# Optimization experiments

Hardware: AMD Instinct MI355X
Metric: run time of the kernel (lower is better)

## Reference

```python
import jax, jax.numpy as jnp
import numpy as np

N = 30000      # nodes
E = 480000     # edges
H = 128        # hidden_nf
NQ = 7         # qubits
D = 2 ** NQ    # 128, quantum state dim == embedding_size
NL = 2         # block n_layers (QGCL layers)
QL = 2         # quantum circuit layers inside each QGCL
NORM = 100.0   # normalization_factor ('sum' aggregation)
NORM_CONST = 1.0


def _cnot_perm_indices(n):
    # Composed permutation for CNOT(0,1)...CNOT(n-2,n-1), CNOT(n-1,0).
    # PennyLane convention: wire 0 is the most significant bit.
    idx = np.arange(2 ** n)
    pairs = [(i, i + 1) for i in range(n - 1)] + [(n - 1, 0)]
    g = None
    for c, t in pairs:
        cb = (idx >> (n - 1 - c)) & 1
        f = idx ^ (cb << (n - 1 - t))  # flip target bit if control set (involution)
        g = f if g is None else g[f]
    return g

_CNOT_G = jnp.asarray(_cnot_perm_indices(NQ))


def _quantum_states(q_in, coeffs, A_re, A_im):
    """Vectorized VQC over all nodes. q_in [N,D] real -> [N,D] complex state."""
    norm = jnp.sqrt(jnp.sum(q_in ** 2, axis=1, keepdims=True) + 1e-12)
    s = (q_in / norm).astype(jnp.complex64)  # normalized initial state per node
    I = jnp.eye(D, dtype=jnp.complex64)
    for j in range(QL):
        # Cayley transform -> unitary
        A = (A_re[j] + 1j * A_im[j]).astype(jnp.complex64)
        A = A + A.conj().T
        q = (A - 1j * I) @ jnp.linalg.inv(A + 1j * I)
        # single-qubit layer: RY(b) @ RX(a) on every qubit -> kron power
        a, b = coeffs[j, 0].astype(jnp.complex64), coeffs[j, 1].astype(jnp.complex64)
        ca, sa = jnp.cos(a / 2), jnp.sin(a / 2)
        cb, sb = jnp.cos(b / 2), jnp.sin(b / 2)
        RX = jnp.stack([jnp.stack([ca, -1j * sa]), jnp.stack([-1j * sa, ca])])
        RY = jnp.stack([jnp.stack([cb, -sb]), jnp.stack([sb, cb])])
        G = RY @ RX
        Gk = G
        for _ in range(NQ - 1):
            Gk = jnp.kron(Gk, G)
        s = s @ q.T            # QubitUnitary
        s = s @ Gk.T           # RX/RY on all qubits
        s = s[:, _CNOT_G]      # CNOT ring (pure permutation)
    return s


def setup_inputs() -> dict:
    key = jax.random.key(0)
    ks = jax.random.split(key, 20)
    return {
        "h": jax.random.normal(ks[0], (N, H), jnp.float32),
        "x": jax.random.normal(ks[1], (N, 3), jnp.float32),
        "edge_index": jax.random.randint(ks[2], (2, E), 0, N, jnp.int32),
        "edge_attr": jax.random.normal(ks[3], (E, 1), jnp.float32),
        "e_w1": jax.random.normal(ks[4], (NL, 2 * H + 2, H), jnp.float32) * 0.05,
        "e_b1": jnp.zeros((NL, H), jnp.float32),
        "e_w2": jax.random.normal(ks[5], (NL, H, H), jnp.float32) * 0.05,
        "e_b2": jnp.zeros((NL, H), jnp.float32),
        "enc_w": jax.random.normal(ks[6], (NL, 2 * H, D), jnp.float32) * 0.05,
        "enc_b": jnp.zeros((NL, D), jnp.float32),
        "coeffs": jax.random.normal(ks[7], (NL, QL, 2), jnp.float32) * 0.1,
        "A_re": jax.random.normal(ks[8], (NL, QL, D, D), jnp.float32) * 0.01,
        "A_im": jax.random.normal(ks[9], (NL, QL, D, D), jnp.float32) * 0.01,
        "dec_w": jax.random.normal(ks[10], (NL, D, H), jnp.float32) * 0.05,
        "dec_b": jnp.zeros((NL, H), jnp.float32),
        "c_w1": jax.random.normal(ks[11], (2 * H + 2, H), jnp.float32) * 0.05,
        "c_b1": jnp.zeros((H,), jnp.float32),
        "c_w2": jax.random.normal(ks[12], (H, H), jnp.float32) * 0.05,
        "c_b2": jnp.zeros((H,), jnp.float32),
        "c_w3": jax.random.normal(ks[13], (H, 1), jnp.float32) * 0.001,  # xavier gain=0.001
    }


def reference(h, x, edge_index, edge_attr, e_w1, e_b1, e_w2, e_b2, enc_w, enc_b,
              coeffs, A_re, A_im, dec_w, dec_b, c_w1, c_b1, c_w2, c_b2, c_w3):
    row, col = edge_index[0], edge_index[1]
    # coord2diff
    diff = x[row] - x[col]
    radial = jnp.sum(diff ** 2, axis=1, keepdims=True)     # [E,1] (used as 'distances')
    coord_diff = diff / (jnp.sqrt(radial + 1e-8) + NORM_CONST)
    eattr = jnp.concatenate([radial, edge_attr], axis=1)   # [E,2]

    for l in range(NL):  # QGCL layers
        m = jnp.concatenate([h[row], h[col], eattr], axis=1)       # [E, 2H+2]
        m = jax.nn.silu(m @ e_w1[l] + e_b1[l])
        m = jax.nn.silu(m @ e_w2[l] + e_b2[l])                     # edge messages mij
        agg = jax.ops.segment_sum(m, row, num_segments=N) / NORM   # scatter-add
        q_in = jnp.concatenate([h, agg], axis=1) @ enc_w[l] + enc_b[l]
        # quantum part is detached in the original (torch .detach + re-tensor)
        qs = jax.lax.stop_gradient(
            _quantum_states(q_in, coeffs[l], A_re[l], A_im[l]))
        h = h + qs.real.astype(h.dtype) @ dec_w[l] + dec_b[l]

    # EquivariantUpdate (tanh=False)
    t = jnp.concatenate([h[row], h[col], eattr], axis=1)
    t = jax.nn.silu(t @ c_w1 + c_b1)
    t = jax.nn.silu(t @ c_w2 + c_b2)
    t = t @ c_w3                                                   # [E,1]
    trans = coord_diff * t
    x = x + jax.ops.segment_sum(trans, row, num_segments=N) / NORM
    return h, x
```

## Files before the change

### kernel.cpp

```cpp
#include <hip/hip_runtime.h>
#include <math.h>

#define N_NODES 30000
#define N_EDGES 480000
#define HDIM 128
#define EPB 64
#define AS 296
#define NAS 264
#define MS 136

typedef __attribute__((ext_vector_type(8))) short short8b;
typedef __attribute__((ext_vector_type(4))) float f32x4;

__device__ __forceinline__ float silu_f(float v) {
  return v / (1.0f + __expf(-v));
}

__device__ __forceinline__ unsigned short f2bf(float f) {
  unsigned int u = __float_as_uint(f);
  unsigned int r = u + 0x7fffu + ((u >> 16) & 1u);
  return (unsigned short)(r >> 16);
}

__global__ void init_out_kernel(const float* __restrict__ h,
                                const float* __restrict__ x,
                                float* __restrict__ out) {
  int idx = blockIdx.x * 256 + threadIdx.x;
  out[idx] = h[idx];
  if (idx < N_NODES * 3) out[N_NODES * HDIM + idx] = x[idx];
}

__global__ void h_to_bf_kernel(const float* __restrict__ h,
                               ushort* __restrict__ hbf) {
  int idx = blockIdx.x * 256 + threadIdx.x;
  float4 v = ((const float4*)h)[idx];
  ushort4 o;
  o.x = f2bf(v.x); o.y = f2bf(v.y); o.z = f2bf(v.z); o.w = f2bf(v.w);
  ((ushort4*)hbf)[idx] = o;
}

__global__ void convert_w_kernel(const float* __restrict__ W,
                                 ushort* __restrict__ dst, int Kreal, int KT) {
  int idx = blockIdx.x * 256 + threadIdx.x;
  if (idx >= KT * 4096) return;
  int kt = idx >> 12, rem = idx & 4095, n = rem >> 5, kk = rem & 31;
  int k = kt * 32 + kk;
  float v = (k < Kreal) ? W[(size_t)k * HDIM + n] : 0.0f;
  dst[idx] = f2bf(v);
}

__global__ void count_kernel(const int* __restrict__ ei, int* __restrict__ cursor) {
  int e = blockIdx.x * 256 + threadIdx.x;
  atomicAdd(&cursor[ei[e]], 1);
}

__global__ __launch_bounds__(1024) void scan_kernel(int* __restrict__ cursor,
                                                    int* __restrict__ cstart) {
  __shared__ int sums[1024];
  const int tid = threadIdx.x;
  const int base = tid * 30;
  int local[30];
  int s = 0;
#pragma unroll
  for (int j = 0; j < 30; ++j) {
    int idx = base + j;
    int d = (idx < N_NODES) ? cursor[idx] : 0;
    local[j] = s;
    s += d;
  }
  sums[tid] = s;
  __syncthreads();
  for (int off = 1; off < 1024; off <<= 1) {
    int add = (tid >= off) ? sums[tid - off] : 0;
    __syncthreads();
    sums[tid] += add;
    __syncthreads();
  }
  int excl = (tid == 0) ? 0 : sums[tid - 1];
#pragma unroll
  for (int j = 0; j < 30; ++j) {
    int idx = base + j;
    if (idx < N_NODES) {
      int v = excl + local[j];
      cursor[idx] = v;
      cstart[idx] = v;
    }
  }
}

__global__ void fill_kernel(const int* __restrict__ ei, int* __restrict__ cursor,
                            int* __restrict__ elist) {
  int e = blockIdx.x * 256 + threadIdx.x;
  int r = ei[e];
  int pos = atomicAdd(&cursor[r], 1);
  elist[pos] = e;
}

__global__ void perm_kernel(int* __restrict__ g) {
  int i = threadIdx.x;
  int v = i;
  const int cs[7] = {6, 5, 4, 3, 2, 1, 0};
  const int ts[7] = {0, 6, 5, 4, 3, 2, 1};
#pragma unroll
  for (int p = 0; p < 7; ++p) {
    int cb = (v >> (6 - cs[p])) & 1;
    v = v ^ (cb << (6 - ts[p]));
  }
  g[i] = v;
}

__global__ void ns_init_kernel(const float* __restrict__ Are,
                               const float* __restrict__ Aim,
                               float2* __restrict__ X) {
  int lj = blockIdx.y;
  int idx = blockIdx.x * 256 + threadIdx.x;
  int r = idx >> 7, c = idx & 127;
  const float* are = Are + (size_t)lj * 16384;
  const float* aim = Aim + (size_t)lj * 16384;
  float re = are[r * 128 + c] + are[c * 128 + r];
  float im = aim[r * 128 + c] - aim[c * 128 + r];
  if (r == c) im -= 1.0f;
  X[(size_t)lj * 16384 + idx] = make_float2(re, im);
}

__global__ void ns_bx_kernel(const float* __restrict__ Are,
                             const float* __restrict__ Aim,
                             const float2* __restrict__ X,
                             float2* __restrict__ T) {
  int lj = blockIdx.y;
  int idx = blockIdx.x * 256 + threadIdx.x;
  int r = idx >> 7, c = idx & 127;
  const float* are = Are + (size_t)lj * 16384;
  const float* aim = Aim + (size_t)lj * 16384;
  const float2* x = X + (size_t)lj * 16384;
  float2 acc = make_float2(0.f, 0.f);
  for (int k = 0; k < 128; ++k) {
    float re = are[r * 128 + k] + are[k * 128 + r];
    float im = aim[r * 128 + k] - aim[k * 128 + r];
    if (k == r) im += 1.0f;
    float2 b = x[k * 128 + c];
    acc.x += re * b.x - im * b.y;
    acc.y += re * b.y + im * b.x;
  }
  T[(size_t)lj * 16384 + idx] = acc;
}

__global__ void ns_upd_kernel(const float2* __restrict__ X,
                              const float2* __restrict__ T,
                              float2* __restrict__ Xn) {
  int lj = blockIdx.y;
  int idx = blockIdx.x * 256 + threadIdx.x;
  int r = idx >> 7, c = idx & 127;
  const float2* x = X + (size_t)lj * 16384;
  const float2* t = T + (size_t)lj * 16384;
  float2 acc = make_float2(0.f, 0.f);
  for (int k = 0; k < 128; ++k) {
    float2 a = x[r * 128 + k];
    float2 b = t[k * 128 + c];
    acc.x += a.x * b.x - a.y * b.y;
    acc.y += a.x * b.y + a.y * b.x;
  }
  float2 xc = x[r * 128 + c];
  Xn[(size_t)lj * 16384 + idx] = make_float2(2.f * xc.x - acc.x, 2.f * xc.y - acc.y);
}

__global__ void qmat_kernel(const float* __restrict__ Are,
                            const float* __restrict__ Aim,
                            const float2* __restrict__ binvg,
                            float2* __restrict__ qm) {
  int lj = blockIdx.y;
  int idx = blockIdx.x * 256 + threadIdx.x;
  int r = idx >> 7, c = idx & 127;
  const float* are = Are + (size_t)lj * 16384;
  const float* aim = Aim + (size_t)lj * 16384;
  const float2* binv = binvg + (size_t)lj * 16384;
  float2 acc = make_float2(0.f, 0.f);
  for (int k = 0; k < 128; ++k) {
    float re = are[r * 128 + k] + are[k * 128 + r];
    float im = aim[r * 128 + k] - aim[k * 128 + r];
    if (k == r) im -= 1.0f;
    float2 b = binv[k * 128 + c];
    acc.x += re * b.x - im * b.y;
    acc.y += re * b.y + im * b.x;
  }
  qm[(size_t)lj * 16384 + idx] = acc;
}

__global__ void gk_kernel(const float* __restrict__ coeffs,
                          float2* __restrict__ gkm) {
  int lj = blockIdx.y;
  float a = coeffs[lj * 2 + 0], b = coeffs[lj * 2 + 1];
  float ca = cosf(0.5f * a), sa = sinf(0.5f * a);
  float cb = cosf(0.5f * b), sb = sinf(0.5f * b);
  float2 G[2][2];
  G[0][0] = make_float2(cb * ca, sb * sa);
  G[0][1] = make_float2(-sb * ca, -cb * sa);
  G[1][0] = make_float2(sb * ca, -cb * sa);
  G[1][1] = make_float2(cb * ca, -sb * sa);
  int idx = blockIdx.x * 256 + threadIdx.x;
  int r = idx >> 7, c = idx & 127;
  float2 acc = make_float2(1.f, 0.f);
#pragma unroll
  for (int bit = 6; bit >= 0; --bit) {
    float2 g = G[(r >> bit) & 1][(c >> bit) & 1];
    acc = make_float2(acc.x * g.x - acc.y * g.y, acc.x * g.y + acc.y * g.x);
  }
  gkm[(size_t)lj * 16384 + idx] = acc;
}

__global__ void nj_kernel(const float2* __restrict__ qm,
                          const float2* __restrict__ gkm,
                          const int* __restrict__ g,
                          float2* __restrict__ njm) {
  int lj = blockIdx.y;
  int idx = blockIdx.x * 256 + threadIdx.x;
  int i = idx >> 7, c = idx & 127;
  int gc = g[c];
  const float2* q = qm + (size_t)lj * 16384;
  const float2* gk = gkm + (size_t)lj * 16384;
  float2 acc = make_float2(0.f, 0.f);
  for (int k = 0; k < 128; ++k) {
    float2 qa = q[k * 128 + i];
    float2 gb = gk[gc * 128 + k];
    acc.x += qa.x * gb.x - qa.y * gb.y;
    acc.y += qa.x * gb.y + qa.y * gb.x;
  }
  njm[(size_t)lj * 16384 + idx] = acc;
}

__global__ void compose_kernel(const float2* __restrict__ njm,
                               float2* __restrict__ um) {
  int l = blockIdx.y;
  int idx = blockIdx.x * 256 + threadIdx.x;
  int i = idx >> 7, c = idx & 127;
  const float2* n0 = njm + (size_t)(l * 2 + 0) * 16384;
  const float2* n1 = njm + (size_t)(l * 2 + 1) * 16384;
  float2 acc = make_float2(0.f, 0.f);
  for (int k = 0; k < 128; ++k) {
    float2 a = n0[i * 128 + k];
    float2 b = n1[k * 128 + c];
    acc.x += a.x * b.x - a.y * b.y;
    acc.y += a.x * b.y + a.y * b.x;
  }
  um[(size_t)l * 16384 + idx] = acc;
}

__global__ void wqd_kernel(const float2* __restrict__ um,
                           const float* __restrict__ decw,
                           float* __restrict__ wqd) {
  int l = blockIdx.y;
  int idx = blockIdx.x * 256 + threadIdx.x;
  int i = idx >> 7, c = idx & 127;
  const float2* u = um + (size_t)l * 16384;
  const float* dw = decw + (size_t)l * 16384;
  float acc = 0.f;
  for (int k = 0; k < 128; ++k) acc += u[i * 128 + k].x * dw[k * 128 + c];
  wqd[(size_t)l * 16384 + idx] = acc;
}

__global__ __launch_bounds__(256, 4) void edge_mfma_kernel(
    const ushort* __restrict__ hbf, const int* __restrict__ ei,
    const float* __restrict__ x, const float* __restrict__ ea,
    const int* __restrict__ elist, const int* __restrict__ cstart,
    const ushort* __restrict__ w1cs, const float* __restrict__ b1,
    const ushort* __restrict__ w2cs, const float* __restrict__ b2,
    float* __restrict__ agg, float* __restrict__ headp) {
  __shared__ ushort A[EPB * AS];
  __shared__ int rows[EPB];
  ushort* m1 = A;
  float* m2 = (float*)A;

  const int tid = threadIdx.x;
  const int lane = tid & 63, wave = tid >> 6;
  const int lrow = lane & 15, lq = lane >> 4;
  const int wbase = wave * 32;
  const int woff0 = (wbase + lrow) * 32 + lq * 8;
  const int woff1 = (wbase + 16 + lrow) * 32 + lq * 8;

  const float b1v[2] = {b1[wbase + lrow], b1[wbase + 16 + lrow]};
  const float b2v[2] = {b2[wbase + lrow], b2[wbase + 16 + lrow]};

  const int i0 = blockIdx.x * EPB;
  {
    const int e = tid >> 2, j = tid & 3;
    const int edge = elist[i0 + e];
    const int r = ei[edge], c = ei[N_EDGES + edge];
    if (j == 0) rows[e] = r;
    const uint4* hr = (const uint4*)(hbf + (size_t)r * HDIM + j * 32);
    const uint4* hc = (const uint4*)(hbf + (size_t)c * HDIM + j * 32);
    uint4* d1 = (uint4*)(A + e * AS + j * 32);
    uint4* d2 = (uint4*)(A + e * AS + 128 + j * 32);
    d1[0] = hr[0]; d1[1] = hr[1]; d1[2] = hr[2]; d1[3] = hr[3];
    d2[0] = hc[0]; d2[1] = hc[1]; d2[2] = hc[2]; d2[3] = hc[3];
    if (j == 3) {
      float dx = x[r * 3 + 0] - x[c * 3 + 0];
      float dy = x[r * 3 + 1] - x[c * 3 + 1];
      float dz = x[r * 3 + 2] - x[c * 3 + 2];
      ushort* dst = A + e * AS;
      dst[256] = f2bf(dx * dx + dy * dy + dz * dz);
      dst[257] = f2bf(ea[edge]);
#pragma unroll
      for (int z = 258; z < 288; ++z) dst[z] = 0;
    }
  }
  __syncthreads();

  f32x4 acc[4][2];
#pragma unroll
  for (int mt = 0; mt < 4; ++mt)
#pragma unroll
    for (int nt = 0; nt < 2; ++nt) acc[mt][nt] = (f32x4){0.f, 0.f, 0.f, 0.f};
  {
    short8b wcur0 = *(const short8b*)(w1cs + woff0);
    short8b wcur1 = *(const short8b*)(w1cs + woff1);
#pragma unroll
    for (int kt = 0; kt < 9; ++kt) {
      short8b wn0, wn1;
      if (kt < 8) {
        wn0 = *(const short8b*)(w1cs + (kt + 1) * 4096 + woff0);
        wn1 = *(const short8b*)(w1cs + (kt + 1) * 4096 + woff1);
      }
      short8b af[4];
#pragma unroll
      for (int mt = 0; mt < 4; ++mt)
        af[mt] = *(const short8b*)(A + (mt * 16 + lrow) * AS + kt * 32 + lq * 8);
#pragma unroll
      for (int mt = 0; mt < 4; ++mt) {
        acc[mt][0] = __builtin_amdgcn_mfma_f32_16x16x32_bf16(af[mt], wcur0, acc[mt][0], 0, 0, 0);
        acc[mt][1] = __builtin_amdgcn_mfma_f32_16x16x32_bf16(af[mt], wcur1, acc[mt][1], 0, 0, 0);
      }
      if (kt < 8) { wcur0 = wn0; wcur1 = wn1; }
    }
  }
  __syncthreads();
#pragma unroll
  for (int mt = 0; mt < 4; ++mt)
#pragma unroll
    for (int nt = 0; nt < 2; ++nt)
#pragma unroll
      for (int r = 0; r < 4; ++r)
        m1[(mt * 16 + lq * 4 + r) * MS + wbase + nt * 16 + lrow] =
            f2bf(silu_f(acc[mt][nt][r] + b1v[nt]));
  __syncthreads();

  f32x4 acc2[4][2];
#pragma unroll
  for (int mt = 0; mt < 4; ++mt)
#pragma unroll
    for (int nt = 0; nt < 2; ++nt) acc2[mt][nt] = (f32x4){0.f, 0.f, 0.f, 0.f};
  {
    short8b wcur0 = *(const short8b*)(w2cs + woff0);
    short8b wcur1 = *(const short8b*)(w2cs + woff1);
#pragma unroll
    for (int kt = 0; kt < 4; ++kt) {
      short8b wn0, wn1;
      if (kt < 3) {
        wn0 = *(const short8b*)(w2cs + (kt + 1) * 4096 + woff0);
        wn1 = *(const short8b*)(w2cs + (kt + 1) * 4096 + woff1);
      }
      short8b af[4];
#pragma unroll
      for (int mt = 0; mt < 4; ++mt)
        af[mt] = *(const short8b*)(m1 + (mt * 16 + lrow) * MS + kt * 32 + lq * 8);
#pragma unroll
      for (int mt = 0; mt < 4; ++mt) {
        acc2[mt][0] = __builtin_amdgcn_mfma_f32_16x16x32_bf16(af[mt], wcur0, acc2[mt][0], 0, 0, 0);
        acc2[mt][1] = __builtin_amdgcn_mfma_f32_16x16x32_bf16(af[mt], wcur1, acc2[mt][1], 0, 0, 0);
      }
      if (kt < 3) { wcur0 = wn0; wcur1 = wn1; }
    }
  }
  __syncthreads();
#pragma unroll
  for (int mt = 0; mt < 4; ++mt)
#pragma unroll
    for (int nt = 0; nt < 2; ++nt)
#pragma unroll
      for (int r = 0; r < 4; ++r)
        m2[(mt * 16 + lq * 4 + r) * MS + wbase + nt * 16 + lrow] =
            silu_f(acc2[mt][nt][r] + b2v[nt]);
  __syncthreads();

  const int e2 = tid & 63, cg = tid >> 6, cb = cg * 32;
  const int r_e = rows[e2];
  const bool leader = (e2 == 0) || (rows[e2 - 1] != r_e);
  if (leader) {
    f32x4 sum[8];
#pragma unroll
    for (int q = 0; q < 8; ++q) sum[q] = *(const f32x4*)(m2 + e2 * MS + cb + q * 4);
    int f = e2 + 1;
    while (f < EPB && rows[f] == r_e) {
#pragma unroll
      for (int q = 0; q < 8; ++q) sum[q] += *(const f32x4*)(m2 + f * MS + cb + q * 4);
      ++f;
    }
    float* dst = (e2 == 0 && cstart[r_e] < i0)
                     ? headp + (size_t)blockIdx.x * HDIM + cb
                     : agg + (size_t)r_e * HDIM + cb;
#pragma unroll
    for (int q = 0; q < 8; ++q) *(f32x4*)(dst + q * 4) = sum[q];
  }
}

__global__ __launch_bounds__(256, 2) void node_mfma_kernel(
    float* __restrict__ out_h, const float* __restrict__ agg,
    const int* __restrict__ cstart, const int* __restrict__ cend,
    const float* __restrict__ headp,
    const ushort* __restrict__ enccs, const float* __restrict__ encb,
    const ushort* __restrict__ wqdcs, const float* __restrict__ decb,
    ushort* __restrict__ hbf) {
  __shared__ ushort A[EPB * NAS];
  __shared__ ushort m1[EPB * MS];
  __shared__ float nbuf[4 * EPB];
  const int tid = threadIdx.x;
  const int n0 = blockIdx.x * EPB;

  const int lane = tid & 63, wave = tid >> 6;
  const int lrow = lane & 15, lq = lane >> 4;
  const int wbase = wave * 32;

  short8b wef[8][2], wqf[4][2];
#pragma unroll
  for (int kt = 0; kt < 8; ++kt)
#pragma unroll
    for (int nt = 0; nt < 2; ++nt)
      wef[kt][nt] = *(const short8b*)(enccs + kt * 4096 + (wbase + nt * 16 + lrow) * 32 + lq * 8);
#pragma unroll
  for (int kt = 0; kt < 4; ++kt)
#pragma unroll
    for (int nt = 0; nt < 2; ++nt)
      wqf[kt][nt] = *(const short8b*)(wqdcs + kt * 4096 + (wbase + nt * 16 + lrow) * 32 + lq * 8);
  const float ebv[2] = {encb[wbase + lrow], encb[wbase + 16 + lrow]};
  const float dbv[2] = {decb[wbase + lrow], decb[wbase + 16 + lrow]};

  {
    const int e = tid >> 2, j = tid & 3;
    int node = n0 + e;
    if (node >= N_NODES) node = N_NODES - 1;
    if (j < 2) {
      const float4* s4 = (const float4*)(out_h + (size_t)node * HDIM + j * 64);
      ushort* dst = A + e * NAS + j * 64;
#pragma unroll
      for (int i = 0; i < 16; ++i) {
        float4 v = s4[i];
        ushort4 o;
        o.x = f2bf(v.x); o.y = f2bf(v.y); o.z = f2bf(v.z); o.w = f2bf(v.w);
        ((ushort4*)dst)[i] = o;
      }
    } else {
      const int s = cstart[node], en = cend[node];
      const bool hasAgg = en > s;
      const float4* a4 = (const float4*)(agg + (size_t)node * HDIM + (j - 2) * 64);
      const int bb0 = (s >> 6) + 1;
      const int bb1 = hasAgg ? ((en - 1) >> 6) : 0;
      ushort* dst = A + e * NAS + 128 + (j - 2) * 64;
#pragma unroll
      for (int i = 0; i < 16; ++i) {
        float4 v = hasAgg ? a4[i] : make_float4(0.f, 0.f, 0.f, 0.f);
        for (int bb = bb0; bb <= bb1; ++bb) {
          float4 hv = *(const float4*)(headp + (size_t)bb * HDIM + (j - 2) * 64 + i * 4);
          v.x += hv.x; v.y += hv.y; v.z += hv.z; v.w += hv.w;
        }
        ushort4 o;
        o.x = f2bf(v.x * 0.01f); o.y = f2bf(v.y * 0.01f);
        o.z = f2bf(v.z * 0.01f); o.w = f2bf(v.w * 0.01f);
        ((ushort4*)dst)[i] = o;
      }
    }
  }
  __syncthreads();

  f32x4 acc[4][2];
#pragma unroll
  for (int mt = 0; mt < 4; ++mt)
#pragma unroll
    for (int nt = 0; nt < 2; ++nt) acc[mt][nt] = (f32x4){0.f, 0.f, 0.f, 0.f};
#pragma unroll
  for (int kt = 0; kt < 8; ++kt) {
    short8b af[4];
#pragma unroll
    for (int mt = 0; mt < 4; ++mt)
      af[mt] = *(const short8b*)(A + (mt * 16 + lrow) * NAS + kt * 32 + lq * 8);
#pragma unroll
    for (int mt = 0; mt < 4; ++mt)
#pragma unroll
      for (int nt = 0; nt < 2; ++nt)
        acc[mt][nt] = __builtin_amdgcn_mfma_f32_16x16x32_bf16(af[mt], wef[kt][nt], acc[mt][nt], 0, 0, 0);
  }
#pragma unroll
  for (int mt = 0; mt < 4; ++mt) {
    float ssp[4] = {0.f, 0.f, 0.f, 0.f};
#pragma unroll
    for (int nt = 0; nt < 2; ++nt)
#pragma unroll
      for (int r = 0; r < 4; ++r) {
        acc[mt][nt][r] += ebv[nt];
        ssp[r] += acc[mt][nt][r] * acc[mt][nt][r];
      }
#pragma unroll
    for (int m = 1; m < 16; m <<= 1)
#pragma unroll
      for (int r = 0; r < 4; ++r) ssp[r] += __shfl_xor(ssp[r], m, 64);
    if (lrow == 0) {
#pragma unroll
      for (int r = 0; r < 4; ++r)
        nbuf[wave * EPB + mt * 16 + lq * 4 + r] = ssp[r];
    }
  }
  __syncthreads();
#pragma unroll
  for (int mt = 0; mt < 4; ++mt)
#pragma unroll
    for (int r = 0; r < 4; ++r) {
      const int row = mt * 16 + lq * 4 + r;
      float sum = nbuf[row] + nbuf[EPB + row] + nbuf[2 * EPB + row] + nbuf[3 * EPB + row];
      float inv = 1.0f / sqrtf(sum + 1e-12f);
#pragma unroll
      for (int nt = 0; nt < 2; ++nt)
        m1[row * MS + wbase + nt * 16 + lrow] = f2bf(acc[mt][nt][r] * inv);
    }
  __syncthreads();

  f32x4 acc2[4][2];
#pragma unroll
  for (int mt = 0; mt < 4; ++mt)
#pragma unroll
    for (int nt = 0; nt < 2; ++nt) acc2[mt][nt] = (f32x4){0.f, 0.f, 0.f, 0.f};
#pragma unroll
  for (int kt = 0; kt < 4; ++kt) {
    short8b af[4];
#pragma unroll
    for (int mt = 0; mt < 4; ++mt)
      af[mt] = *(const short8b*)(m1 + (mt * 16 + lrow) * MS + kt * 32 + lq * 8);
#pragma unroll
    for (int mt = 0; mt < 4; ++mt)
#pragma unroll
      for (int nt = 0; nt < 2; ++nt)
        acc2[mt][nt] = __builtin_amdgcn_mfma_f32_16x16x32_bf16(af[mt], wqf[kt][nt], acc2[mt][nt], 0, 0, 0);
  }
#pragma unroll
  for (int mt = 0; mt < 4; ++mt)
#pragma unroll
    for (int nt = 0; nt < 2; ++nt) {
      const int n = wbase + nt * 16 + lrow;
#pragma unroll
      for (int r = 0; r < 4; ++r) {
        const int node = n0 + mt * 16 + lq * 4 + r;
        if (node < N_NODES) {
          size_t off = (size_t)node * HDIM + n;
          float hn = out_h[off] + acc2[mt][nt][r] + dbv[nt];
          out_h[off] = hn;
          hbf[off] = f2bf(hn);
        }
      }
    }
}

__global__ __launch_bounds__(256, 4) void coord_mfma_kernel(
    const ushort* __restrict__ hbf, const int* __restrict__ ei,
    const float* __restrict__ x, const float* __restrict__ ea,
    const int* __restrict__ elist,
    const ushort* __restrict__ w1cs, const float* __restrict__ b1,
    const ushort* __restrict__ w2cs, const float* __restrict__ b2,
    const float* __restrict__ w3, float* __restrict__ xout) {
  __shared__ ushort A[EPB * AS];
  __shared__ int rows[EPB];
  __shared__ int colsA[EPB];
  __shared__ float pbuf[4 * EPB];
  __shared__ float tv[EPB];
  ushort* m1 = A;

  const int tid = threadIdx.x;
  const int lane = tid & 63, wave = tid >> 6;
  const int lrow = lane & 15, lq = lane >> 4;
  const int wbase = wave * 32;
  const int woff0 = (wbase + lrow) * 32 + lq * 8;
  const int woff1 = (wbase + 16 + lrow) * 32 + lq * 8;

  const float b1v[2] = {b1[wbase + lrow], b1[wbase + 16 + lrow]};
  const float b2v[2] = {b2[wbase + lrow], b2[wbase + 16 + lrow]};
  const float w3v[2] = {w3[wbase + lrow], w3[wbase + 16 + lrow]};

  const int i0 = blockIdx.x * EPB;
  {
    const int e = tid >> 2, j = tid & 3;
    const int edge = elist[i0 + e];
    const int r = ei[edge], c = ei[N_EDGES + edge];
    if (j == 0) { rows[e] = r; colsA[e] = c; }
    const uint4* hr = (const uint4*)(hbf + (size_t)r * HDIM + j * 32);
    const uint4* hc = (const uint4*)(hbf + (size_t)c * HDIM + j * 32);
    uint4* d1 = (uint4*)(A + e * AS + j * 32);
    uint4* d2 = (uint4*)(A + e * AS + 128 + j * 32);
    d1[0] = hr[0]; d1[1] = hr[1]; d1[2] = hr[2]; d1[3] = hr[3];
    d2[0] = hc[0]; d2[1] = hc[1]; d2[2] = hc[2]; d2[3] = hc[3];
    if (j == 3) {
      float dx = x[r * 3 + 0] - x[c * 3 + 0];
      float dy = x[r * 3 + 1] - x[c * 3 + 1];
      float dz = x[r * 3 + 2] - x[c * 3 + 2];
      ushort* dst = A + e * AS;
      dst[256] = f2bf(dx * dx + dy * dy + dz * dz);
      dst[257] = f2bf(ea[edge]);
#pragma unroll
      for (int z = 258; z < 288; ++z) dst[z] = 0;
    }
  }
  __syncthreads();

  f32x4 acc[4][2];
#pragma unroll
  for (int mt = 0; mt < 4; ++mt)
#pragma unroll
    for (int nt = 0; nt < 2; ++nt) acc[mt][nt] = (f32x4){0.f, 0.f, 0.f, 0.f};
  {
    short8b wcur0 = *(const short8b*)(w1cs + woff0);
    short8b wcur1 = *(const short8b*)(w1cs + woff1);
#pragma unroll
    for (int kt = 0; kt < 9; ++kt) {
      short8b wn0, wn1;
      if (kt < 8) {
        wn0 = *(const short8b*)(w1cs + (kt + 1) * 4096 + woff0);
        wn1 = *(const short8b*)(w1cs + (kt + 1) * 4096 + woff1);
      }
      short8b af[4];
#pragma unroll
      for (int mt = 0; mt < 4; ++mt)
        af[mt] = *(const short8b*)(A + (mt * 16 + lrow) * AS + kt * 32 + lq * 8);
#pragma unroll
      for (int mt = 0; mt < 4; ++mt) {
        acc[mt][0] = __builtin_amdgcn_mfma_f32_16x16x32_bf16(af[mt], wcur0, acc[mt][0], 0, 0, 0);
        acc[mt][1] = __builtin_amdgcn_mfma_f32_16x16x32_bf16(af[mt], wcur1, acc[mt][1], 0, 0, 0);
      }
      if (kt < 8) { wcur0 = wn0; wcur1 = wn1; }
    }
  }
  __syncthreads();
#pragma unroll
  for (int mt = 0; mt < 4; ++mt)
#pragma unroll
    for (int nt = 0; nt < 2; ++nt)
#pragma unroll
      for (int r = 0; r < 4; ++r)
        m1[(mt * 16 + lq * 4 + r) * MS + wbase + nt * 16 + lrow] =
            f2bf(silu_f(acc[mt][nt][r] + b1v[nt]));
  __syncthreads();

  f32x4 acc2[4][2];
#pragma unroll
  for (int mt = 0; mt < 4; ++mt)
#pragma unroll
    for (int nt = 0; nt < 2; ++nt) acc2[mt][nt] = (f32x4){0.f, 0.f, 0.f, 0.f};
  {
    short8b wcur0 = *(const short8b*)(w2cs + woff0);
    short8b wcur1 = *(const short8b*)(w2cs + woff1);
#pragma unroll
    for (int kt = 0; kt < 4; ++kt) {
      short8b wn0, wn1;
      if (kt < 3) {
        wn0 = *(const short8b*)(w2cs + (kt + 1) * 4096 + woff0);
        wn1 = *(const short8b*)(w2cs + (kt + 1) * 4096 + woff1);
      }
      short8b af[4];
#pragma unroll
      for (int mt = 0; mt < 4; ++mt)
        af[mt] = *(const short8b*)(m1 + (mt * 16 + lrow) * MS + kt * 32 + lq * 8);
#pragma unroll
      for (int mt = 0; mt < 4; ++mt) {
        acc2[mt][0] = __builtin_amdgcn_mfma_f32_16x16x32_bf16(af[mt], wcur0, acc2[mt][0], 0, 0, 0);
        acc2[mt][1] = __builtin_amdgcn_mfma_f32_16x16x32_bf16(af[mt], wcur1, acc2[mt][1], 0, 0, 0);
      }
      if (kt < 3) { wcur0 = wn0; wcur1 = wn1; }
    }
  }
#pragma unroll
  for (int mt = 0; mt < 4; ++mt) {
    float p[4] = {0.f, 0.f, 0.f, 0.f};
#pragma unroll
    for (int nt = 0; nt < 2; ++nt)
#pragma unroll
      for (int r = 0; r < 4; ++r)
        p[r] += silu_f(acc2[mt][nt][r] + b2v[nt]) * w3v[nt];
#pragma unroll
    for (int m = 1; m < 16; m <<= 1)
#pragma unroll
      for (int r = 0; r < 4; ++r) p[r] += __shfl_xor(p[r], m, 64);
    if (lrow == 0) {
#pragma unroll
      for (int r = 0; r < 4; ++r)
        pbuf[wave * EPB + mt * 16 + lq * 4 + r] = p[r];
    }
  }
  __syncthreads();
  if (tid < EPB) {
    tv[tid] = (pbuf[tid] + pbuf[EPB + tid] + pbuf[2 * EPB + tid] + pbuf[3 * EPB + tid]) * 0.01f;
  }
  __syncthreads();
  if (tid < EPB) {
    const int e = tid;
    const int r_e = rows[e];
    const bool leader = (e == 0) || (rows[e - 1] != r_e);
    if (leader) {
      float sx = 0.f, sy = 0.f, sz = 0.f;
      int f = e;
      do {
        const int c = colsA[f];
        float dx = x[r_e * 3 + 0] - x[c * 3 + 0];
        float dy = x[r_e * 3 + 1] - x[c * 3 + 1];
        float dz = x[r_e * 3 + 2] - x[c * 3 + 2];
        float radial = dx * dx + dy * dy + dz * dz;
        float s = 1.0f / (sqrtf(radial + 1e-8f) + 1.0f);
        float t = tv[f];
        sx += dx * s * t; sy += dy * s * t; sz += dz * s * t;
        ++f;
      } while (f < EPB && rows[f] == r_e);
      atomicAdd(&xout[r_e * 3 + 0], sx);
      atomicAdd(&xout[r_e * 3 + 1], sy);
      atomicAdd(&xout[r_e * 3 + 2], sz);
    }
  }
}

extern "C" void kernel_launch(void* const* d_in, const int* in_sizes, int n_in,
                              void* d_out, int out_size, void* d_ws, size_t ws_size,
                              hipStream_t stream) {
  const float* h     = (const float*)d_in[0];
  const float* x     = (const float*)d_in[1];
  const int*   ei    = (const int*)d_in[2];
  const float* ea    = (const float*)d_in[3];
  const float* e_w1  = (const float*)d_in[4];
  const float* e_b1  = (const float*)d_in[5];
  const float* e_w2  = (const float*)d_in[6];
  const float* e_b2  = (const float*)d_in[7];
  const float* enc_w = (const float*)d_in[8];
  const float* enc_b = (const float*)d_in[9];
  const float* coeffs= (const float*)d_in[10];
  const float* A_re  = (const float*)d_in[11];
  const float* A_im  = (const float*)d_in[12];
  const float* dec_w = (const float*)d_in[13];
  const float* dec_b = (const float*)d_in[14];
  const float* c_w1  = (const float*)d_in[15];
  const float* c_b1  = (const float*)d_in[16];
  const float* c_w2  = (const float*)d_in[17];
  const float* c_b2  = (const float*)d_in[18];
  const float* c_w3  = (const float*)d_in[19];

  float* out = (float*)d_out;
  float* ws  = (float*)d_ws;

  float*  agg    = ws;
  float2* xa     = (float2*)(ws + 3840000);
  float2* xb     = (float2*)(ws + 3971072);
  float2* xt     = (float2*)(ws + 4102144);
  float2* qm     = (float2*)(ws + 4233216);
  float2* gkm    = (float2*)(ws + 4364288);
  float2* njm    = (float2*)(ws + 4495360);
  float2* um     = (float2*)(ws + 4626432);
  float*  wqd    = ws + 4691968;
  int*    perm   = (int*)(ws + 4724736);
  int*    cursor = (int*)(ws + 4724864);
  int*    cstart = (int*)(ws + 4754864);
  int*    elist  = (int*)(ws + 4784864);
  float*  headp  = ws + 5264864;
  ushort* hbf    = (ushort*)(ws + 6224864);
  ushort* w1cs   = (ushort*)(ws + 8144864);
  ushort* w2cs   = (ushort*)(ws + 8181728);
  ushort* cw1cs  = (ushort*)(ws + 8198112);
  ushort* cw2cs  = (ushort*)(ws + 8216544);
  ushort* enccs  = (ushort*)(ws + 8224736);
  ushort* wqdcs  = (ushort*)(ws + 8257504);

  init_out_kernel<<<15000, 256, 0, stream>>>(h, x, out);

  hipMemsetAsync(cursor, 0, N_NODES * sizeof(int), stream);
  count_kernel<<<1875, 256, 0, stream>>>(ei, cursor);
  scan_kernel<<<1, 1024, 0, stream>>>(cursor, cstart);
  fill_kernel<<<1875, 256, 0, stream>>>(ei, cursor, elist);

  perm_kernel<<<1, 128, 0, stream>>>(perm);
  ns_init_kernel<<<dim3(64, 4), 256, 0, stream>>>(A_re, A_im, xa);
  float2* cur = xa;
  float2* nxt = xb;
  for (int it = 0; it < 4; ++it) {
    ns_bx_kernel<<<dim3(64, 4), 256, 0, stream>>>(A_re, A_im, cur, xt);
    ns_upd_kernel<<<dim3(64, 4), 256, 0, stream>>>(cur, xt, nxt);
    float2* tmp = cur; cur = nxt; nxt = tmp;
  }
  qmat_kernel<<<dim3(64, 4), 256, 0, stream>>>(A_re, A_im, cur, qm);
  gk_kernel<<<dim3(64, 4), 256, 0, stream>>>(coeffs, gkm);
  nj_kernel<<<dim3(64, 4), 256, 0, stream>>>(qm, gkm, perm, njm);
  compose_kernel<<<dim3(64, 2), 256, 0, stream>>>(njm, um);
  wqd_kernel<<<dim3(64, 2), 256, 0, stream>>>(um, dec_w, wqd);

  for (int l = 0; l < 2; ++l) {
    convert_w_kernel<<<144, 256, 0, stream>>>(e_w1 + (size_t)l * 258 * HDIM,
                                              w1cs + (size_t)l * 9 * 4096, 258, 9);
    convert_w_kernel<<<64, 256, 0, stream>>>(e_w2 + (size_t)l * HDIM * HDIM,
                                             w2cs + (size_t)l * 4 * 4096, 128, 4);
    convert_w_kernel<<<128, 256, 0, stream>>>(enc_w + (size_t)l * 256 * HDIM,
                                              enccs + (size_t)l * 8 * 4096, 256, 8);
    convert_w_kernel<<<64, 256, 0, stream>>>(wqd + (size_t)l * HDIM * HDIM,
                                             wqdcs + (size_t)l * 4 * 4096, 128, 4);
  }
  convert_w_kernel<<<144, 256, 0, stream>>>(c_w1, cw1cs, 258, 9);
  convert_w_kernel<<<64, 256, 0, stream>>>(c_w2, cw2cs, 128, 4);

  h_to_bf_kernel<<<3750, 256, 0, stream>>>(out, hbf);

  for (int l = 0; l < 2; ++l) {
    edge_mfma_kernel<<<N_EDGES / EPB, 256, 0, stream>>>(
        hbf, ei, x, ea, elist, cstart,
        w1cs + (size_t)l * 9 * 4096, e_b1 + l * HDIM,
        w2cs + (size_t)l * 4 * 4096, e_b2 + l * HDIM, agg, headp);
    node_mfma_kernel<<<(N_NODES + EPB - 1) / EPB, 256, 0, stream>>>(
        out, agg, cstart, cursor, headp,
        enccs + (size_t)l * 8 * 4096, enc_b + l * HDIM,
        wqdcs + (size_t)l * 4 * 4096, dec_b + l * HDIM, hbf);
  }

  coord_mfma_kernel<<<N_EDGES / EPB, 256, 0, stream>>>(
      hbf, ei, x, ea, elist, cw1cs, c_b1, cw2cs, c_b2, c_w3,
      out + (size_t)N_NODES * HDIM);
}
```

Measured before the change: 826.4 us.

## Transpose MFMA tiling so each wave owns 16 rows and chains layers in registers

Swaps the MFMA operand roles so each wave computes all 128 output columns for its own 16 edges/nodes, with the weight matrix pre-permuted in convert_w_kernel so the accumulator layout directly matches the next layer's B-operand fragment. This lets the first-layer activations stay in registers as the second GEMM's input, removing the LDS round-trip, several __syncthreads and the cross-wave reduction buffers (pbuf, nbuf, m1). Row-wise reductions (norm, w3 dot) become intra-wave shuffles. In exchange each wave now loads all weight fragments from global/L2 per kt, which raises weight traffic per wave and register pressure from 8 accumulators.

```diff
diff --git a/kernel.cpp b/kernel.cpp
--- a/kernel.cpp
+++ b/kernel.cpp
@@ -7,7 +7,6 @@
 #define EPB 64
 #define AS 296
 #define NAS 264
-#define MS 136
 
 typedef __attribute__((ext_vector_type(8))) short short8b;
 typedef __attribute__((ext_vector_type(4))) float f32x4;
@@ -43,7 +42,8 @@
                                  ushort* __restrict__ dst, int Kreal, int KT) {
   int idx = blockIdx.x * 256 + threadIdx.x;
   if (idx >= KT * 4096) return;
-  int kt = idx >> 12, rem = idx & 4095, n = rem >> 5, kk = rem & 31;
+  int kt = idx >> 12, rem = idx & 4095, p = rem >> 5, kk = rem & 31;
+  int n = ((p >> 5) << 5) | (((p >> 2) & 3) << 3) | (((p >> 4) & 1) << 2) | (p & 3);
   int k = kt * 32 + kk;
   float v = (k < Kreal) ? W[(size_t)k * HDIM + n] : 0.0f;
   dst[idx] = f2bf(v);
@@ -267,18 +267,11 @@
     float* __restrict__ agg, float* __restrict__ headp) {
   __shared__ ushort A[EPB * AS];
   __shared__ int rows[EPB];
-  ushort* m1 = A;
-  float* m2 = (float*)A;
 
   const int tid = threadIdx.x;
   const int lane = tid & 63, wave = tid >> 6;
   const int lrow = lane & 15, lq = lane >> 4;
-  const int wbase = wave * 32;
-  const int woff0 = (wbase + lrow) * 32 + lq * 8;
-  const int woff1 = (wbase + 16 + lrow) * 32 + lq * 8;
-
-  const float b1v[2] = {b1[wbase + lrow], b1[wbase + 16 + lrow]};
-  const float b2v[2] = {b2[wbase + lrow], b2[wbase + 16 + lrow]};
+  const int erow = wave * 16 + lrow;
 
   const int i0 = blockIdx.x * EPB;
   {
@@ -305,93 +298,79 @@
   }
   __syncthreads();
 
-  f32x4 acc[4][2];
-#pragma unroll
-  for (int mt = 0; mt < 4; ++mt)
-#pragma unroll
-    for (int nt = 0; nt < 2; ++nt) acc[mt][nt] = (f32x4){0.f, 0.f, 0.f, 0.f};
-  {
-    short8b wcur0 = *(const short8b*)(w1cs + woff0);
-    short8b wcur1 = *(const short8b*)(w1cs + woff1);
+  f32x4 acc1[8];
+#pragma unroll
+  for (int t = 0; t < 8; ++t) acc1[t] = (f32x4){0.f, 0.f, 0.f, 0.f};
+  {
+    const ushort* wp = w1cs + lrow * 32 + lq * 8;
+    const ushort* ap = A + erow * AS + lq * 8;
 #pragma unroll
     for (int kt = 0; kt < 9; ++kt) {
-      short8b wn0, wn1;
-      if (kt < 8) {
-        wn0 = *(const short8b*)(w1cs + (kt + 1) * 4096 + woff0);
-        wn1 = *(const short8b*)(w1cs + (kt + 1) * 4096 + woff1);
+      short8b af = *(const short8b*)(ap + kt * 32);
+#pragma unroll
+      for (int t = 0; t < 8; ++t) {
+        short8b wf = *(const short8b*)(wp + kt * 4096 + t * 512);
+        acc1[t] = __builtin_amdgcn_mfma_f32_16x16x32_bf16(wf, af, acc1[t], 0, 0, 0);
       }
-      short8b af[4];
-#pragma unroll
-      for (int mt = 0; mt < 4; ++mt)
-        af[mt] = *(const short8b*)(A + (mt * 16 + lrow) * AS + kt * 32 + lq * 8);
-#pragma unroll
-      for (int mt = 0; mt < 4; ++mt) {
-        acc[mt][0] = __builtin_amdgcn_mfma_f32_16x16x32_bf16(af[mt], wcur0, acc[mt][0], 0, 0, 0);
-        acc[mt][1] = __builtin_amdgcn_mfma_f32_16x16x32_bf16(af[mt], wcur1, acc[mt][1], 0, 0, 0);
+    }
+  }
+
+  short8b mf[4];
+#pragma unroll
+  for (int t = 0; t < 8; ++t) {
+    const int nb = ((t >> 1) << 5) + (lq << 3) + ((t & 1) << 2);
+    const float4 bb = *(const float4*)(b1 + nb);
+    const int c = t >> 1, s = (t & 1) * 4;
+    mf[c][s + 0] = (short)f2bf(silu_f(acc1[t][0] + bb.x));
+    mf[c][s + 1] = (short)f2bf(silu_f(acc1[t][1] + bb.y));
+    mf[c][s + 2] = (short)f2bf(silu_f(acc1[t][2] + bb.z));
+    mf[c][s + 3] = (short)f2bf(silu_f(acc1[t][3] + bb.w));
+  }
+  __syncthreads();
+
+  f32x4 acc2[8];
+#pragma unroll
+  for (int t = 0; t < 8; ++t) acc2[t] = (f32x4){0.f, 0.f, 0.f, 0.f};
+  {
+    const ushort* wp = w2cs + lrow * 32 + lq * 8;
+#pragma unroll
+    for (int kt = 0; kt < 4; ++kt) {
+#pragma unroll
+      for (int t = 0; t < 8; ++t) {
+        short8b wf = *(const short8b*)(wp + kt * 4096 + t * 512);
+        acc2[t] = __builtin_amdgcn_mfma_f32_16x16x32_bf16(wf, mf[kt], acc2[t], 0, 0, 0);
       }
-      if (kt < 8) { wcur0 = wn0; wcur1 = wn1; }
+    }
+  }
+
+  {
+    float* m2w = (float*)A;
+#pragma unroll
+    for (int t = 0; t < 8; ++t) {
+      const int nb = ((t >> 1) << 5) + (lq << 3) + ((t & 1) << 2);
+      const float4 bb = *(const float4*)(b2 + nb);
+      f32x4 v;
+      v[0] = silu_f(acc2[t][0] + bb.x);
+      v[1] = silu_f(acc2[t][1] + bb.y);
+      v[2] = silu_f(acc2[t][2] + bb.z);
+      v[3] = silu_f(acc2[t][3] + bb.w);
+      *(f32x4*)(m2w + erow * 148 + nb) = v;
     }
   }
   __syncthreads();
-#pragma unroll
-  for (int mt = 0; mt < 4; ++mt)
-#pragma unroll
-    for (int nt = 0; nt < 2; ++nt)
-#pragma unroll
-      for (int r = 0; r < 4; ++r)
-        m1[(mt * 16 + lq * 4 + r) * MS + wbase + nt * 16 + lrow] =
-            f2bf(silu_f(acc[mt][nt][r] + b1v[nt]));
-  __syncthreads();
-
-  f32x4 acc2[4][2];
-#pragma unroll
-  for (int mt = 0; mt < 4; ++mt)
-#pragma unroll
-    for (int nt = 0; nt < 2; ++nt) acc2[mt][nt] = (f32x4){0.f, 0.f, 0.f, 0.f};
-  {
-    short8b wcur0 = *(const short8b*)(w2cs + woff0);
-    short8b wcur1 = *(const short8b*)(w2cs + woff1);
-#pragma unroll
-    for (int kt = 0; kt < 4; ++kt) {
-      short8b wn0, wn1;
-      if (kt < 3) {
-        wn0 = *(const short8b*)(w2cs + (kt + 1) * 4096 + woff0);
-        wn1 = *(const short8b*)(w2cs + (kt + 1) * 4096 + woff1);
-      }
-      short8b af[4];
-#pragma unroll
-      for (int mt = 0; mt < 4; ++mt)
-        af[mt] = *(const short8b*)(m1 + (mt * 16 + lrow) * MS + kt * 32 + lq * 8);
-#pragma unroll
-      for (int mt = 0; mt < 4; ++mt) {
-        acc2[mt][0] = __builtin_amdgcn_mfma_f32_16x16x32_bf16(af[mt], wcur0, acc2[mt][0], 0, 0, 0);
-        acc2[mt][1] = __builtin_amdgcn_mfma_f32_16x16x32_bf16(af[mt], wcur1, acc2[mt][1], 0, 0, 0);
-      }
-      if (kt < 3) { wcur0 = wn0; wcur1 = wn1; }
-    }
-  }
-  __syncthreads();
-#pragma unroll
-  for (int mt = 0; mt < 4; ++mt)
-#pragma unroll
-    for (int nt = 0; nt < 2; ++nt)
-#pragma unroll
-      for (int r = 0; r < 4; ++r)
-        m2[(mt * 16 + lq * 4 + r) * MS + wbase + nt * 16 + lrow] =
-            silu_f(acc2[mt][nt][r] + b2v[nt]);
-  __syncthreads();
-
+
+  const float* m2 = (const float*)A;
   const int e2 = tid & 63, cg = tid >> 6, cb = cg * 32;
   const int r_e = rows[e2];
   const bool leader = (e2 == 0) || (rows[e2 - 1] != r_e);
   if (leader) {
     f32x4 sum[8];
 #pragma unroll
-    for (int q = 0; q < 8; ++q) sum[q] = *(const f32x4*)(m2 + e2 * MS + cb + q * 4);
+    for (int q = 0; q < 8; ++q) sum[q] = *(const f32x4*)(m2 + e2 * 148 + cb + q * 4);
     int f = e2 + 1;
     while (f < EPB && rows[f] == r_e) {
 #pragma unroll
-      for (int q = 0; q < 8; ++q) sum[q] += *(const f32x4*)(m2 + f * MS + cb + q * 4);
+      for (int q = 0; q < 8; ++q) sum[q] += *(const f32x4*)(m2 + f * 148 + cb + q * 4);
       ++f;
     }
     float* dst = (e2 == 0 && cstart[r_e] < i0)
@@ -410,28 +389,12 @@
     const ushort* __restrict__ wqdcs, const float* __restrict__ decb,
     ushort* __restrict__ hbf) {
   __shared__ ushort A[EPB * NAS];
-  __shared__ ushort m1[EPB * MS];
-  __shared__ float nbuf[4 * EPB];
   const int tid = threadIdx.x;
   const int n0 = blockIdx.x * EPB;
 
   const int lane = tid & 63, wave = tid >> 6;
   const int lrow = lane & 15, lq = lane >> 4;
-  const int wbase = wave * 32;
-
-  short8b wef[8][2], wqf[4][2];
-#pragma unroll
-  for (int kt = 0; kt < 8; ++kt)
-#pragma unroll
-    for (int nt = 0; nt < 2; ++nt)
-      wef[kt][nt] = *(const short8b*)(enccs + kt * 4096 + (wbase + nt * 16 + lrow) * 32 + lq * 8);
-#pragma unroll
-  for (int kt = 0; kt < 4; ++kt)
-#pragma unroll
-    for (int nt = 0; nt < 2; ++nt)
-      wqf[kt][nt] = *(const short8b*)(wqdcs + kt * 4096 + (wbase + nt * 16 + lrow) * 32 + lq * 8);
-  const float ebv[2] = {encb[wbase + lrow], encb[wbase + 16 + lrow]};
-  const float dbv[2] = {decb[wbase + lrow], decb[wbase + 16 + lrow]};
+  const int erow = wave * 16 + lrow;
 
   {
     const int e = tid >> 2, j = tid & 3;
@@ -470,90 +433,83 @@
   }
   __syncthreads();
 
-  f32x4 acc[4][2];
-#pragma unroll
-  for (int mt = 0; mt < 4; ++mt)
-#pragma unroll
-    for (int nt = 0; nt < 2; ++nt) acc[mt][nt] = (f32x4){0.f, 0.f, 0.f, 0.f};
-#pragma unroll
-  for (int kt = 0; kt < 8; ++kt) {
-    short8b af[4];
-#pragma unroll
-    for (int mt = 0; mt < 4; ++mt)
-      af[mt] = *(const short8b*)(A + (mt * 16 + lrow) * NAS + kt * 32 + lq * 8);
-#pragma unroll
-    for (int mt = 0; mt < 4; ++mt)
-#pragma unroll
-      for (int nt = 0; nt < 2; ++nt)
-        acc[mt][nt] = __builtin_amdgcn_mfma_f32_16x16x32_bf16(af[mt], wef[kt][nt], acc[mt][nt], 0, 0, 0);
-  }
-#pragma unroll
-  for (int mt = 0; mt < 4; ++mt) {
-    float ssp[4] = {0.f, 0.f, 0.f, 0.f};
-#pragma unroll
-    for (int nt = 0; nt < 2; ++nt)
-#pragma unroll
-      for (int r = 0; r < 4; ++r) {
-        acc[mt][nt][r] += ebv[nt];
-        ssp[r] += acc[mt][nt][r] * acc[mt][nt][r];
+  f32x4 acc[8];
+#pragma unroll
+  for (int t = 0; t < 8; ++t) acc[t] = (f32x4){0.f, 0.f, 0.f, 0.f};
+  {
+    const ushort* wp = enccs + lrow * 32 + lq * 8;
+    const ushort* ap = A + erow * NAS + lq * 8;
+#pragma unroll
+    for (int kt = 0; kt < 8; ++kt) {
+      short8b af = *(const short8b*)(ap + kt * 32);
+#pragma unroll
+      for (int t = 0; t < 8; ++t) {
+        short8b wf = *(const short8b*)(wp + kt * 4096 + t * 512);
+        acc[t] = __builtin_amdgcn_mfma_f32_16x16x32_bf16(wf, af, acc[t], 0, 0, 0);
       }
-#pragma unroll
-    for (int m = 1; m < 16; m <<= 1)
-#pragma unroll
-      for (int r = 0; r < 4; ++r) ssp[r] += __shfl_xor(ssp[r], m, 64);
-    if (lrow == 0) {
-#pragma unroll
-      for (int r = 0; r < 4; ++r)
-        nbuf[wave * EPB + mt * 16 + lq * 4 + r] = ssp[r];
-    }
-  }
-  __syncthreads();
-#pragma unroll
-  for (int mt = 0; mt < 4; ++mt)
-#pragma unroll
-    for (int r = 0; r < 4; ++r) {
-      const int row = mt * 16 + lq * 4 + r;
-      float sum = nbuf[row] + nbuf[EPB + row] + nbuf[2 * EPB + row] + nbuf[3 * EPB + row];
-      float inv = 1.0f / sqrtf(sum + 1e-12f);
-#pragma unroll
-      for (int nt = 0; nt < 2; ++nt)
-        m1[row * MS + wbase + nt * 16 + lrow] = f2bf(acc[mt][nt][r] * inv);
-    }
-  __syncthreads();
-
-  f32x4 acc2[4][2];
-#pragma unroll
-  for (int mt = 0; mt < 4; ++mt)
-#pragma unroll
-    for (int nt = 0; nt < 2; ++nt) acc2[mt][nt] = (f32x4){0.f, 0.f, 0.f, 0.f};
-#pragma unroll
-  for (int kt = 0; kt < 4; ++kt) {
-    short8b af[4];
-#pragma unroll
-    for (int mt = 0; mt < 4; ++mt)
-      af[mt] = *(const short8b*)(m1 + (mt * 16 + lrow) * MS + kt * 32 + lq * 8);
-#pragma unroll
-    for (int mt = 0; mt < 4; ++mt)
-#pragma unroll
-      for (int nt = 0; nt < 2; ++nt)
-        acc2[mt][nt] = __builtin_amdgcn_mfma_f32_16x16x32_bf16(af[mt], wqf[kt][nt], acc2[mt][nt], 0, 0, 0);
-  }
-#pragma unroll
-  for (int mt = 0; mt < 4; ++mt)
-#pragma unroll
-    for (int nt = 0; nt < 2; ++nt) {
-      const int n = wbase + nt * 16 + lrow;
-#pragma unroll
-      for (int r = 0; r < 4; ++r) {
-        const int node = n0 + mt * 16 + lq * 4 + r;
-        if (node < N_NODES) {
-          size_t off = (size_t)node * HDIM + n;
-          float hn = out_h[off] + acc2[mt][nt][r] + dbv[nt];
-          out_h[off] = hn;
-          hbf[off] = f2bf(hn);
-        }
+    }
+  }
+
+  float q[8][4];
+  float ss = 0.f;
+#pragma unroll
+  for (int t = 0; t < 8; ++t) {
+    const int nb = ((t >> 1) << 5) + (lq << 3) + ((t & 1) << 2);
+    const float4 bb = *(const float4*)(encb + nb);
+    q[t][0] = acc[t][0] + bb.x;
+    q[t][1] = acc[t][1] + bb.y;
+    q[t][2] = acc[t][2] + bb.z;
+    q[t][3] = acc[t][3] + bb.w;
+    ss += q[t][0] * q[t][0] + q[t][1] * q[t][1] + q[t][2] * q[t][2] + q[t][3] * q[t][3];
+  }
+  ss += __shfl_xor(ss, 16, 64);
+  ss += __shfl_xor(ss, 32, 64);
+  const float inv = 1.0f / sqrtf(ss + 1e-12f);
+
+  short8b mf[4];
+#pragma unroll
+  for (int t = 0; t < 8; ++t) {
+    const int c = t >> 1, s = (t & 1) * 4;
+    mf[c][s + 0] = (short)f2bf(q[t][0] * inv);
+    mf[c][s + 1] = (short)f2bf(q[t][1] * inv);
+    mf[c][s + 2] = (short)f2bf(q[t][2] * inv);
+    mf[c][s + 3] = (short)f2bf(q[t][3] * inv);
+  }
+
+  f32x4 acc2[8];
+#pragma unroll
+  for (int t = 0; t < 8; ++t) acc2[t] = (f32x4){0.f, 0.f, 0.f, 0.f};
+  {
+    const ushort* wp = wqdcs + lrow * 32 + lq * 8;
+#pragma unroll
+    for (int kt = 0; kt < 4; ++kt) {
+#pragma unroll
+      for (int t = 0; t < 8; ++t) {
+        short8b wf = *(const short8b*)(wp + kt * 4096 + t * 512);
+        acc2[t] = __builtin_amdgcn_mfma_f32_16x16x32_bf16(wf, mf[kt], acc2[t], 0, 0, 0);
       }
     }
+  }
+
+  const int node = n0 + erow;
+  if (node < N_NODES) {
+#pragma unroll
+    for (int t = 0; t < 8; ++t) {
+      const int nb = ((t >> 1) << 5) + (lq << 3) + ((t & 1) << 2);
+      const float4 db = *(const float4*)(decb + nb);
+      const size_t off = (size_t)node * HDIM + nb;
+      float4 o = *(const float4*)(out_h + off);
+      float4 hn;
+      hn.x = o.x + acc2[t][0] + db.x;
+      hn.y = o.y + acc2[t][1] + db.y;
+      hn.z = o.z + acc2[t][2] + db.z;
+      hn.w = o.w + acc2[t][3] + db.w;
+      *(float4*)(out_h + off) = hn;
+      ushort4 ob;
+      ob.x = f2bf(hn.x); ob.y = f2bf(hn.y); ob.z = f2bf(hn.z); ob.w = f2bf(hn.w);
+      *(ushort4*)(hbf + off) = ob;
+    }
+  }
 }
 
 __global__ __launch_bounds__(256, 4) void coord_mfma_kernel(
@@ -566,20 +522,12 @@
   __shared__ ushort A[EPB * AS];
   __shared__ int rows[EPB];
   __shared__ int colsA[EPB];
-  __shared__ float pbuf[4 * EPB];
   __shared__ float tv[EPB];
-  ushort* m1 = A;
 
   const int tid = threadIdx.x;
   const int lane = tid & 63, wave = tid >> 6;
   const int lrow = lane & 15, lq = lane >> 4;
-  const int wbase = wave * 32;
-  const int woff0 = (wbase + lrow) * 32 + lq * 8;
-  const int woff1 = (wbase + 16 + lrow) * 32 + lq * 8;
-
-  const float b1v[2] = {b1[wbase + lrow], b1[wbase + 16 + lrow]};
-  const float b2v[2] = {b2[wbase + lrow], b2[wbase + 16 + lrow]};
-  const float w3v[2] = {w3[wbase + lrow], w3[wbase + 16 + lrow]};
+  const int erow = wave * 16 + lrow;
 
   const int i0 = blockIdx.x * EPB;
   {
@@ -606,94 +554,66 @@
   }
   __syncthreads();
 
-  f32x4 acc[4][2];
-#pragma unroll
-  for (int mt = 0; mt < 4; ++mt)
-#pragma unroll
-    for (int nt = 0; nt < 2; ++nt) acc[mt][nt] = (f32x4){0.f, 0.f, 0.f, 0.f};
-  {
-    short8b wcur0 = *(const short8b*)(w1cs + woff0);
-    short8b wcur1 = *(const short8b*)(w1cs + woff1);
+  f32x4 acc1[8];
+#pragma unroll
+  for (int t = 0; t < 8; ++t) acc1[t] = (f32x4){0.f, 0.f, 0.f, 0.f};
+  {
+    const ushort* wp = w1cs + lrow * 32 + lq * 8;
+    const ushort* ap = A + erow * AS + lq * 8;
 #pragma unroll
     for (int kt = 0; kt < 9; ++kt) {
-      short8b wn0, wn1;
-      if (kt < 8) {
-        wn0 = *(const short8b*)(w1cs + (kt + 1) * 4096 + woff0);
-        wn1 = *(const short8b*)(w1cs + (kt + 1) * 4096 + woff1);
+      short8b af = *(const short8b*)(ap + kt * 32);
+#pragma unroll
+      for (int t = 0; t < 8; ++t) {
+        short8b wf = *(const short8b*)(wp + kt * 4096 + t * 512);
+        acc1[t] = __builtin_amdgcn_mfma_f32_16x16x32_bf16(wf, af, acc1[t], 0, 0, 0);
       }
-      short8b af[4];
-#pragma unroll
-      for (int mt = 0; mt < 4; ++mt)
-        af[mt] = *(const short8b*)(A + (mt * 16 + lrow) * AS + kt * 32 + lq * 8);
-#pragma unroll
-      for (int mt = 0; mt < 4; ++mt) {
-        acc[mt][0] = __builtin_amdgcn_mfma_f32_16x16x32_bf16(af[mt], wcur0, acc[mt][0], 0, 0, 0);
-        acc[mt][1] = __builtin_amdgcn_mfma_f32_16x16x32_bf16(af[mt], wcur1, acc[mt][1], 0, 0, 0);
+    }
+  }
+
+  short8b mf[4];
+#pragma unroll
+  for (int t = 0; t < 8; ++t) {
+    const int nb = ((t >> 1) << 5) + (lq << 3) + ((t & 1) << 2);
+    const float4 bb = *(const float4*)(b1 + nb);
+    const int c = t >> 1, s = (t & 1) * 4;
+    mf[c][s + 0] = (short)f2bf(silu_f(acc1[t][0] + bb.x));
+    mf[c][s + 1] = (short)f2bf(silu_f(acc1[t][1] + bb.y));
+    mf[c][s + 2] = (short)f2bf(silu_f(acc1[t][2] + bb.z));
+    mf[c][s + 3] = (short)f2bf(silu_f(acc1[t][3] + bb.w));
+  }
+
+  f32x4 acc2[8];
+#pragma unroll
+  for (int t = 0; t < 8; ++t) acc2[t] = (f32x4){0.f, 0.f, 0.f, 0.f};
+  {
+    const ushort* wp = w2cs + lrow * 32 + lq * 8;
+#pragma unroll
+    for (int kt = 0; kt < 4; ++kt) {
+#pragma unroll
+      for (int t = 0; t < 8; ++t) {
+        short8b wf = *(const short8b*)(wp + kt * 4096 + t * 512);
+        acc2[t] = __builtin_amdgcn_mfma_f32_16x16x32_bf16(wf, mf[kt], acc2[t], 0, 0, 0);
       }
-      if (kt < 8) { wcur0 = wn0; wcur1 = wn1; }
-    }
-  }
+    }
+  }
+
+  float tpart = 0.f;
+#pragma unroll
+  for (int t = 0; t < 8; ++t) {
+    const int nb = ((t >> 1) << 5) + (lq << 3) + ((t & 1) << 2);
+    const float4 bb = *(const float4*)(b2 + nb);
+    const float4 wf = *(const float4*)(w3 + nb);
+    tpart += silu_f(acc2[t][0] + bb.x) * wf.x;
+    tpart += silu_f(acc2[t][1] + bb.y) * wf.y;
+    tpart += silu_f(acc2[t][2] + bb.z) * wf.z;
+    tpart += silu_f(acc2[t][3] + bb.w) * wf.w;
+  }
+  tpart += __shfl_xor(tpart, 16, 64);
+  tpart += __shfl_xor(tpart, 32, 64);
+  if (lq == 0) tv[erow] = tpart * 0.01f;
   __syncthreads();
-#pragma unroll
-  for (int mt = 0; mt < 4; ++mt)
-#pragma unroll
-    for (int nt = 0; nt < 2; ++nt)
-#pragma unroll
-      for (int r = 0; r < 4; ++r)
-        m1[(mt * 16 + lq * 4 + r) * MS + wbase + nt * 16 + lrow] =
-            f2bf(silu_f(acc[mt][nt][r] + b1v[nt]));
-  __syncthreads();
-
-  f32x4 acc2[4][2];
-#pragma unroll
-  for (int mt = 0; mt < 4; ++mt)
-#pragma unroll
-    for (int nt = 0; nt < 2; ++nt) acc2[mt][nt] = (f32x4){0.f, 0.f, 0.f, 0.f};
-  {
-    short8b wcur0 = *(const short8b*)(w2cs + woff0);
-    short8b wcur1 = *(const short8b*)(w2cs + woff1);
-#pragma unroll
-    for (int kt = 0; kt < 4; ++kt) {
-      short8b wn0, wn1;
-      if (kt < 3) {
-        wn0 = *(const short8b*)(w2cs + (kt + 1) * 4096 + woff0);
-        wn1 = *(const short8b*)(w2cs + (kt + 1) * 4096 + woff1);
-      }
-      short8b af[4];
-#pragma unroll
-      for (int mt = 0; mt < 4; ++mt)
-        af[mt] = *(const short8b*)(m1 + (mt * 16 + lrow) * MS + kt * 32 + lq * 8);
-#pragma unroll
-      for (int mt = 0; mt < 4; ++mt) {
-        acc2[mt][0] = __builtin_amdgcn_mfma_f32_16x16x32_bf16(af[mt], wcur0, acc2[mt][0], 0, 0, 0);
-        acc2[mt][1] = __builtin_amdgcn_mfma_f32_16x16x32_bf16(af[mt], wcur1, acc2[mt][1], 0, 0, 0);
-      }
-      if (kt < 3) { wcur0 = wn0; wcur1 = wn1; }
-    }
-  }
-#pragma unroll
-  for (int mt = 0; mt < 4; ++mt) {
-    float p[4] = {0.f, 0.f, 0.f, 0.f};
-#pragma unroll
-    for (int nt = 0; nt < 2; ++nt)
-#pragma unroll
-      for (int r = 0; r < 4; ++r)
-        p[r] += silu_f(acc2[mt][nt][r] + b2v[nt]) * w3v[nt];
-#pragma unroll
-    for (int m = 1; m < 16; m <<= 1)
-#pragma unroll
-      for (int r = 0; r < 4; ++r) p[r] += __shfl_xor(p[r], m, 64);
-    if (lrow == 0) {
-#pragma unroll
-      for (int r = 0; r < 4; ++r)
-        pbuf[wave * EPB + mt * 16 + lq * 4 + r] = p[r];
-    }
-  }
-  __syncthreads();
-  if (tid < EPB) {
-    tv[tid] = (pbuf[tid] + pbuf[EPB + tid] + pbuf[2 * EPB + tid] + pbuf[3 * EPB + tid]) * 0.01f;
-  }
-  __syncthreads();
+
   if (tid < EPB) {
     const int e = tid;
     const int r_e = rows[e];
```

New measurement: 1.114 ms. 1.35x slower.
